# Kernel tuning notes

Hardware: AMD Instinct MI355X
Metric: run time of the kernel (lower is better)

The kernel has to match this reference:

```python
import jax, jax.numpy as jnp
import numpy as np

NUM_HEADS = 6
DIM = 192
WS = (2, 6, 12)          # window size (z, h, w)
DATA = (8, 96, 180)      # padded (plev, lat, lon)
SHIFT = (1, 3, 6)


def _position_index(ws):
    Z, H, W = ws
    zi, zj = np.arange(Z), -np.arange(Z) * Z
    hi, hj = np.arange(H), -np.arange(H) * H
    w = np.arange(W)
    c1 = np.stack(np.meshgrid(zi, hi, w, indexing='ij')).reshape(3, -1)
    c2 = np.stack(np.meshgrid(zj, hj, w, indexing='ij')).reshape(3, -1)
    coords = (c1[:, :, None] - c2[:, None, :]).transpose(1, 2, 0).copy()
    coords[:, :, 2] += W - 1
    coords[:, :, 1] *= 2 * W - 1
    coords[:, :, 0] *= (2 * W - 1) * H * H
    return coords.sum(-1).reshape(-1).astype(np.int32)


def _shift_mask(data, ws, ss):
    Z, H, W = data
    img = np.zeros((Z, H, W))
    cnt = 0
    for z in ((0, -ss[0]), (-ss[0], None)):
        for h in ((0, -ss[1]), (-ss[1], None)):
            for w in ((0, None),):  # lam=False: longitude is cyclic, no w split
                img[z[0]:z[1], h[0]:h[1], w[0]:w[1]] = cnt
                cnt += 1
    m = img.reshape(Z // ws[0], ws[0], H // ws[1], ws[1], W // ws[2], ws[2])
    m = m.transpose(0, 2, 4, 1, 3, 5).reshape(-1, ws[0] * ws[1] * ws[2])
    diff = m[:, None, :] - m[:, :, None]
    return np.where(diff != 0, -100.0, 0.0).astype(np.float32)


def setup_inputs() -> dict:
    key = jax.random.key(0)
    ks = jax.random.split(key, 4)
    N = WS[0] * WS[1] * WS[2]                      # 144 tokens / window
    nW = (DATA[0] // WS[0]) * (DATA[1] // WS[1])   # 64 (z,h) window pairs
    wlon = DATA[2] // WS[2]                        # 15 lon windows
    B_ = 1 * nW * wlon                             # 960 total windows (batch=1)
    bias_rows = (2 * WS[2] - 1) * WS[1] ** 2 * WS[0] ** 2  # 3312
    return {
        'x': jax.random.normal(ks[0], (B_, N, DIM), jnp.float32),
        'w1': jax.random.normal(ks[1], (DIM, 3 * DIM), jnp.float32) * 0.02,
        'b1': jnp.zeros((3 * DIM,), jnp.float32),
        'w2': jax.random.normal(ks[2], (DIM, DIM), jnp.float32) * 0.02,
        'b2': jnp.zeros((DIM,), jnp.float32),
        'bias_table': jax.random.normal(ks[3], (bias_rows, nW, NUM_HEADS), jnp.float32) * 0.02,
        'mask': jnp.asarray(_shift_mask(DATA, WS, SHIFT)),
        'position_index': jnp.asarray(_position_index(WS)),
        'batch_size': 1,
    }


def reference(x, w1, b1, w2, b2, bias_table, mask, position_index, batch_size):
    B_, N, C = x.shape
    Ch = C // NUM_HEADS
    scale = Ch ** -0.5
    qkv = (x @ w1 + b1).reshape(B_, N, 3, NUM_HEADS, Ch)
    qkv = jnp.transpose(qkv, (2, 0, 3, 1, 4))      # (3, B_, H, N, Ch)
    q, k, v = qkv[0] * scale, qkv[1], qkv[2]
    attn = jnp.einsum('bhnc,bhmc->bhnm', q, k)      # (B_, H, N, N)
    nW = bias_table.shape[1]
    wlon = B_ // (batch_size * nW)
    # earth-specific bias gather: (N*N,) -> (nW, H, N, N)
    bias = bias_table[position_index].reshape(N, N, nW, NUM_HEADS)
    bias = jnp.transpose(bias, (2, 3, 0, 1))
    attn = attn.reshape(batch_size, nW, wlon, NUM_HEADS, N, N) + bias[None, :, None]
    # shift mask add: (total_windows, N, N) broadcast over batch and heads
    attn = attn.reshape(batch_size, nW * wlon, NUM_HEADS, N, N) + mask[None, :, None]
    attn = jax.nn.softmax(attn.reshape(B_, NUM_HEADS, N, N), axis=-1)
    out = jnp.einsum('bhnm,bhmc->bnhc', attn, v).reshape(B_, N, C)
    return out @ w2 + b2
```

## Files before the change

kernel.cpp:

```cpp
#include <hip/hip_runtime.h>

typedef __attribute__((ext_vector_type(8))) short bf16x8;
typedef __attribute__((ext_vector_type(4))) float f32x4;
typedef unsigned short u16;
typedef unsigned int u32;

#define NTOK 144
#define CDIM 192
#define NH 6
#define CH 32
#define C3 576
#define NWIN 64
#define WLON 15
#define SCALE 0.17677669529663687f
#define LOG2E 1.4426950408889634f

#define OFF_W1T  0u
#define OFF_W2T  221184u
#define OFF_COMB 294912u
#define OFF_Q    16220160u
#define OFF_K    69304320u
#define OFF_V    122388480u

__device__ __forceinline__ u16 f2b(float f){
  u32 u = __float_as_uint(f);
  u32 r = u + 0x7FFFu + ((u >> 16) & 1u);
  return (u16)(r >> 16);
}
__device__ __forceinline__ u32 pk2(float a, float b){
  return (u32)f2b(a) | ((u32)f2b(b) << 16);
}

extern "C" __global__ __launch_bounds__(256) void prep_weights(
    const float* __restrict__ w1, const float* __restrict__ w2,
    u16* __restrict__ w1t, u16* __restrict__ w2t){
  int idx = blockIdx.x * 256 + threadIdx.x;
  if (idx < CDIM * C3){ int k = idx / C3;  int c = idx - k * C3;  w1t[c * CDIM + k] = f2b(w1[idx]); }
  if (idx < CDIM * CDIM){ int k = idx / CDIM; int c = idx - k * CDIM; w2t[c * CDIM + k] = f2b(w2[idx]); }
}

extern "C" __global__ __launch_bounds__(192) void prep_comb(
    const float* __restrict__ bt, const float* __restrict__ mask,
    const int* __restrict__ pidx, u16* __restrict__ comb){
  int nwh = blockIdx.x;
  int nw = nwh / NH, h = nwh - nw * NH;
  int tl = blockIdx.y * 192 + threadIdx.x;
  int ti = tl / 576;
  int rem = tl - ti * 576;
  int nt = rem >> 6, lane = rem & 63;
  int ib = ti * 16 + ((lane >> 4) << 2);
  int j  = nt * 16 + (lane & 15);
  const float* mrow = mask + (size_t)(nw * WLON) * (NTOK * NTOK);
  float v[4];
  #pragma unroll
  for (int r = 0; r < 4; ++r){
    int e = (ib + r) * NTOK + j;
    int pi = pidx[e];
    v[r] = (bt[((size_t)pi * NWIN + nw) * NH + h] + mrow[e]) * LOG2E;
  }
  uint2 out; out.x = pk2(v[0], v[1]); out.y = pk2(v[2], v[3]);
  *reinterpret_cast<uint2*>(comb + ((size_t)nwh * 5184 + tl) * 4) = out;
}

#define BPAD 200
extern "C" __global__ __launch_bounds__(256, 3) void qkv_gemm(
    const float* __restrict__ x, const u16* __restrict__ w1t, const float* __restrict__ b1,
    u16* __restrict__ qw, u16* __restrict__ kw, u16* __restrict__ vw){
  __shared__ u16 Bl[2][64 * BPAD];
  const int tid = threadIdx.x;
  const int wid = tid >> 6, lane = tid & 63, l15 = lane & 15, l4 = lane >> 4;
  const size_t row0 = (size_t)blockIdx.x * 128 + wid * 32;
  const f32x4 zz = {0.f, 0.f, 0.f, 0.f};

  bf16x8 af[2][6];
  #pragma unroll
  for (int mf = 0; mf < 2; ++mf){
    const float* src = x + (row0 + mf * 16 + l15) * CDIM + l4 * 8;
    #pragma unroll
    for (int kk = 0; kk < 6; ++kk){
      float4 f0 = *reinterpret_cast<const float4*>(src + kk * 32);
      float4 f1 = *reinterpret_cast<const float4*>(src + kk * 32 + 4);
      union { bf16x8 v; uint4 u; } cv;
      cv.u.x = pk2(f0.x, f0.y); cv.u.y = pk2(f0.z, f0.w);
      cv.u.z = pk2(f1.x, f1.y); cv.u.w = pk2(f1.z, f1.w);
      af[mf][kk] = cv.v;
    }
  }
  int bw_[2], n0_[2];
  #pragma unroll
  for (int mf = 0; mf < 2; ++mf){
    int t0 = (int)row0 + mf * 16 + l4 * 4;
    bw_[mf] = t0 / NTOK; n0_[mf] = t0 - bw_[mf] * NTOK;
  }

  const int sr = tid >> 2, sq = tid & 3;
  {
    const u16* src = w1t + (size_t)sr * CDIM + sq * 48;
    u16* dst = &Bl[0][sr * BPAD + sq * 48];
    #pragma unroll
    for (int i = 0; i < 48; i += 8)
      *reinterpret_cast<uint4*>(dst + i) = *reinterpret_cast<const uint4*>(src + i);
  }

  int cur = 0;
  #pragma unroll 1
  for (int nt = 0; nt < 9; ++nt){
    __syncthreads();
    if (nt < 8){
      const u16* src = w1t + (size_t)((nt + 1) * 64 + sr) * CDIM + sq * 48;
      u16* dst = &Bl[cur ^ 1][sr * BPAD + sq * 48];
      #pragma unroll
      for (int i = 0; i < 48; i += 8)
        *reinterpret_cast<uint4*>(dst + i) = *reinterpret_cast<const uint4*>(src + i);
    }
    f32x4 acc[2][4];
    #pragma unroll
    for (int mf = 0; mf < 2; ++mf)
      #pragma unroll
      for (int nf = 0; nf < 4; ++nf) acc[mf][nf] = zz;
    #pragma unroll
    for (int kk = 0; kk < 6; ++kk){
      bf16x8 bfr[4];
      #pragma unroll
      for (int nf = 0; nf < 4; ++nf)
        bfr[nf] = *reinterpret_cast<const bf16x8*>(&Bl[cur][(nf * 16 + l15) * BPAD + kk * 32 + l4 * 8]);
      #pragma unroll
      for (int mf = 0; mf < 2; ++mf)
        #pragma unroll
        for (int nf = 0; nf < 4; ++nf)
          acc[mf][nf] = __builtin_amdgcn_mfma_f32_16x16x32_bf16(af[mf][kk], bfr[nf], acc[mf][nf], 0, 0, 0);
    }
    int which = nt / 3;
    #pragma unroll
    for (int nf = 0; nf < 4; ++nf){
      int c = nt * 64 + nf * 16 + l15;
      int rem = c - which * CDIM;
      int hh = rem >> 5, chh = rem & 31;
      float bias = b1[c];
      if (which == 2){
        #pragma unroll
        for (int mf = 0; mf < 2; ++mf){
          uint2 pv;
          pv.x = pk2(acc[mf][nf][0] + bias, acc[mf][nf][1] + bias);
          pv.y = pk2(acc[mf][nf][2] + bias, acc[mf][nf][3] + bias);
          *reinterpret_cast<uint2*>(vw + (((size_t)bw_[mf] * NH + hh) * CH + chh) * NTOK + n0_[mf]) = pv;
        }
      } else {
        u16* base = (which == 0) ? qw : kw;
        float mult = (which == 0) ? (SCALE * LOG2E) : 1.0f;
        #pragma unroll
        for (int mf = 0; mf < 2; ++mf)
          #pragma unroll
          for (int r = 0; r < 4; ++r)
            base[(((size_t)bw_[mf] * NH + hh) * NTOK + n0_[mf] + r) * CH + chh] = f2b((acc[mf][nf][r] + bias) * mult);
      }
    }
    cur ^= 1;
  }
}

extern "C" __global__ __launch_bounds__(512) void attn_kernel(
    const u16* __restrict__ qw, const u16* __restrict__ kw, const u16* __restrict__ vw,
    const u16* __restrict__ comb, float* __restrict__ outbuf){
  __shared__ u16 Pl[8][16][40];
  const int tid = threadIdx.x;
  const int wv = tid >> 6, lane = tid & 63, l15 = lane & 15, l4 = lane >> 4;
  const int gw = blockIdx.x * 8 + wv;
  const int b = gw / NH, h = gw - b * NH;
  const size_t qkbase = ((size_t)b * NH + h) * (NTOK * CH);
  const size_t vbase  = ((size_t)b * NH + h) * (CH * NTOK);
  const u16* cb = comb + ((size_t)((b / WLON) * NH + h)) * (5184 * 4);
  u16* Pw = &Pl[wv][0][0];
  u32* stash32 = reinterpret_cast<u32*>(outbuf);
  const f32x4 zz = {0.f, 0.f, 0.f, 0.f};

  uint2 cc[9];
  #pragma unroll
  for (int nt = 0; nt < 9; ++nt)
    cc[nt] = *reinterpret_cast<const uint2*>(cb + ((size_t)nt * 64 + lane) * 4);

  #pragma unroll 1
  for (int ti = 0; ti < 9; ++ti){
    const int tin = (ti < 8) ? ti + 1 : ti;
    uint2 ccn[9];
    #pragma unroll
    for (int nt = 0; nt < 9; ++nt)
      ccn[nt] = *reinterpret_cast<const uint2*>(cb + ((size_t)(tin * 9 + nt) * 64 + lane) * 4);

    bf16x8 aq = *reinterpret_cast<const bf16x8*>(qw + qkbase + (ti * 16 + l15) * CH + l4 * 8);
    f32x4 s[9];
    #pragma unroll
    for (int nt = 0; nt < 9; ++nt){
      f32x4 cf;
      cf[0] = __uint_as_float(cc[nt].x << 16);
      cf[1] = __uint_as_float(cc[nt].x & 0xFFFF0000u);
      cf[2] = __uint_as_float(cc[nt].y << 16);
      cf[3] = __uint_as_float(cc[nt].y & 0xFFFF0000u);
      bf16x8 bk = *reinterpret_cast<const bf16x8*>(kw + qkbase + (nt * 16 + l15) * CH + l4 * 8);
      s[nt] = __builtin_amdgcn_mfma_f32_16x16x32_bf16(aq, bk, cf, 0, 0, 0);
    }
    float invs[4];
    #pragma unroll
    for (int r = 0; r < 4; ++r){
      float sum = 0.f;
      #pragma unroll
      for (int nt = 0; nt < 9; ++nt){
        float p = exp2f(s[nt][r]);
        s[nt][r] = p; sum += p;
      }
      #pragma unroll
      for (int off = 8; off; off >>= 1) sum += __shfl_xor(sum, off, 16);
      invs[r] = 1.0f / sum;
    }
    f32x4 oe = zz, oo = zz;
    #pragma unroll
    for (int kk = 0; kk < 5; ++kk){
      #pragma unroll
      for (int r = 0; r < 4; ++r){
        Pw[(l4 * 4 + r) * 40 + l15] = f2b(s[2 * kk][r]);
        if (kk < 4) Pw[(l4 * 4 + r) * 40 + 16 + l15] = f2b(s[2 * kk + 1][r]);
      }
      int j0 = kk * 32 + l4 * 8;
      int jc = (j0 < NTOK) ? j0 : 0;
      bf16x8 ap = *reinterpret_cast<const bf16x8*>(Pw + l15 * 40 + l4 * 8);
      bf16x8 bve = *reinterpret_cast<const bf16x8*>(vw + vbase + (size_t)(2 * l15) * NTOK + jc);
      bf16x8 bvo = *reinterpret_cast<const bf16x8*>(vw + vbase + (size_t)(2 * l15 + 1) * NTOK + jc);
      if (j0 >= NTOK) ap = bf16x8{0, 0, 0, 0, 0, 0, 0, 0};
      oe = __builtin_amdgcn_mfma_f32_16x16x32_bf16(ap, bve, oe, 0, 0, 0);
      oo = __builtin_amdgcn_mfma_f32_16x16x32_bf16(ap, bvo, oo, 0, 0, 0);
    }
    #pragma unroll
    for (int r = 0; r < 4; ++r){
      size_t t = (size_t)b * NTOK + ti * 16 + l4 * 4 + r;
      float is = invs[r];
      stash32[t * 192 + 96 + h * 16 + l15] = pk2(oe[r] * is, oo[r] * is);
    }
    #pragma unroll
    for (int nt = 0; nt < 9; ++nt) cc[nt] = ccn[nt];
  }
}

extern "C" __global__ __launch_bounds__(256, 2) void proj_gemm(
    const u16* __restrict__ w2t, const float* __restrict__ b2, float* __restrict__ outbuf){
  const int tid = threadIdx.x;
  const int wid = tid >> 6, lane = tid & 63, l15 = lane & 15, l4 = lane >> 4;
  const int hb = blockIdx.y;
  const f32x4 zz = {0.f, 0.f, 0.f, 0.f};

  bf16x8 bfr[6][6];
  #pragma unroll
  for (int nf = 0; nf < 6; ++nf)
    #pragma unroll
    for (int kk = 0; kk < 6; ++kk)
      bfr[nf][kk] = *reinterpret_cast<const bf16x8*>(
          w2t + (size_t)(hb * 96 + nf * 16 + l15) * CDIM + kk * 32 + l4 * 8);

  const u16* stash = reinterpret_cast<const u16*>(outbuf);
  const size_t rbase = (size_t)blockIdx.x * 256 + wid * 64;

#define LOADA(dst, mt) { \
    const u16* src_ = stash + (rbase + (mt) * 16 + l15) * 384 + 192 + l4 * 8; \
    _Pragma("unroll") \
    for (int kk = 0; kk < 6; ++kk) dst[kk] = *reinterpret_cast<const bf16x8*>(src_ + kk * 32); }

#define COMPUTE(a_, mt) { \
    f32x4 acc[6]; \
    _Pragma("unroll") \
    for (int nf = 0; nf < 6; ++nf) acc[nf] = zz; \
    _Pragma("unroll") \
    for (int kk = 0; kk < 6; ++kk) \
      _Pragma("unroll") \
      for (int nf = 0; nf < 6; ++nf) \
        acc[nf] = __builtin_amdgcn_mfma_f32_16x16x32_bf16(a_[kk], bfr[nf][kk], acc[nf], 0, 0, 0); \
    _Pragma("unroll") \
    for (int nf = 0; nf < 6; ++nf){ \
      int c = hb * 96 + nf * 16 + l15; \
      float bias = b2[c]; \
      _Pragma("unroll") \
      for (int r = 0; r < 4; ++r) \
        outbuf[(rbase + (mt) * 16 + l4 * 4 + r) * CDIM + c] = acc[nf][r] + bias; } }

  bf16x8 a0[6], a1[6];
  LOADA(a0, 0)
  LOADA(a1, 1) COMPUTE(a0, 0)
  LOADA(a0, 2) COMPUTE(a1, 1)
  LOADA(a1, 3) COMPUTE(a0, 2)
  COMPUTE(a1, 3)
#undef LOADA
#undef COMPUTE
}

extern "C" void kernel_launch(void* const* d_in, const int* in_sizes, int n_in,
                              void* d_out, int out_size, void* d_ws, size_t ws_size,
                              hipStream_t stream){
  const float* x    = (const float*)d_in[0];
  const float* w1   = (const float*)d_in[1];
  const float* b1   = (const float*)d_in[2];
  const float* w2   = (const float*)d_in[3];
  const float* b2   = (const float*)d_in[4];
  const float* bt   = (const float*)d_in[5];
  const float* mask = (const float*)d_in[6];
  const int*   pidx = (const int*)d_in[7];
  (void)in_sizes; (void)n_in; (void)out_size; (void)ws_size;

  char* ws = (char*)d_ws;
  u16*   w1t  = (u16*)(ws + OFF_W1T);
  u16*   w2t  = (u16*)(ws + OFF_W2T);
  u16*   comb = (u16*)(ws + OFF_COMB);
  u16*   qw   = (u16*)(ws + OFF_Q);
  u16*   kw   = (u16*)(ws + OFF_K);
  u16*   vw   = (u16*)(ws + OFF_V);
  float* out = (float*)d_out;

  prep_weights<<<dim3(432), dim3(256), 0, stream>>>(w1, w2, w1t, w2t);
  prep_comb<<<dim3(384, 27), dim3(192), 0, stream>>>(bt, mask, pidx, comb);
  qkv_gemm<<<dim3(1080), dim3(256), 0, stream>>>(x, w1t, b1, qw, kw, vw);
  attn_kernel<<<dim3(720), dim3(512), 0, stream>>>(qw, kw, vw, comb, out);
  proj_gemm<<<dim3(540, 2), dim3(256), 0, stream>>>(w2t, b2, out);
}
```

Baseline: 247.2 us.

## Pair adjacent output columns per lane in QKV GEMM and defer weight-tile LDS store

The QKV projection kernel now interleaves the B-tile rows so each lane owns two adjacent output channels, which lets Q/K writes become packed 32-bit stores instead of scattered 16-bit stores. The next weight tile is loaded from global memory into registers at the start of an iteration and written to the alternate LDS buffer only after the MFMAs and epilogue, so global load latency overlaps with compute. The cost is six extra uint4 registers per thread and a changed barrier placement.

```diff
diff --git a/kernel.cpp b/kernel.cpp
--- a/kernel.cpp
+++ b/kernel.cpp
@@ -101,60 +101,74 @@
     for (int i = 0; i < 48; i += 8)
       *reinterpret_cast<uint4*>(dst + i) = *reinterpret_cast<const uint4*>(src + i);
   }
+  __syncthreads();
 
   int cur = 0;
   #pragma unroll 1
   for (int nt = 0; nt < 9; ++nt){
-    __syncthreads();
+    uint4 ld[6];
     if (nt < 8){
       const u16* src = w1t + (size_t)((nt + 1) * 64 + sr) * CDIM + sq * 48;
-      u16* dst = &Bl[cur ^ 1][sr * BPAD + sq * 48];
-      #pragma unroll
-      for (int i = 0; i < 48; i += 8)
-        *reinterpret_cast<uint4*>(dst + i) = *reinterpret_cast<const uint4*>(src + i);
-    }
-    f32x4 acc[2][4];
-    #pragma unroll
-    for (int mf = 0; mf < 2; ++mf)
-      #pragma unroll
-      for (int nf = 0; nf < 4; ++nf) acc[mf][nf] = zz;
+      #pragma unroll
+      for (int i = 0; i < 6; ++i)
+        ld[i] = *reinterpret_cast<const uint4*>(src + i * 8);
+    }
+    f32x4 acc[4][2];
+    #pragma unroll
+    for (int f = 0; f < 4; ++f){ acc[f][0] = zz; acc[f][1] = zz; }
     #pragma unroll
     for (int kk = 0; kk < 6; ++kk){
       bf16x8 bfr[4];
       #pragma unroll
-      for (int nf = 0; nf < 4; ++nf)
-        bfr[nf] = *reinterpret_cast<const bf16x8*>(&Bl[cur][(nf * 16 + l15) * BPAD + kk * 32 + l4 * 8]);
-      #pragma unroll
-      for (int mf = 0; mf < 2; ++mf)
+      for (int f = 0; f < 4; ++f){
+        int brow = (f >> 1) * 32 + 2 * l15 + (f & 1);
+        bfr[f] = *reinterpret_cast<const bf16x8*>(&Bl[cur][brow * BPAD + kk * 32 + l4 * 8]);
+      }
+      #pragma unroll
+      for (int f = 0; f < 4; ++f)
         #pragma unroll
-        for (int nf = 0; nf < 4; ++nf)
-          acc[mf][nf] = __builtin_amdgcn_mfma_f32_16x16x32_bf16(af[mf][kk], bfr[nf], acc[mf][nf], 0, 0, 0);
+        for (int mf = 0; mf < 2; ++mf)
+          acc[f][mf] = __builtin_amdgcn_mfma_f32_16x16x32_bf16(af[mf][kk], bfr[f], acc[f][mf], 0, 0, 0);
     }
     int which = nt / 3;
     #pragma unroll
-    for (int nf = 0; nf < 4; ++nf){
-      int c = nt * 64 + nf * 16 + l15;
-      int rem = c - which * CDIM;
-      int hh = rem >> 5, chh = rem & 31;
-      float bias = b1[c];
+    for (int nf = 0; nf < 2; ++nf){
+      int cbase = nt * 64 + nf * 32;
+      int ce = cbase + 2 * l15;
+      float be = b1[ce], bo = b1[ce + 1];
+      int hh = (cbase >> 5) - which * 6;
       if (which == 2){
         #pragma unroll
         for (int mf = 0; mf < 2; ++mf){
-          uint2 pv;
-          pv.x = pk2(acc[mf][nf][0] + bias, acc[mf][nf][1] + bias);
-          pv.y = pk2(acc[mf][nf][2] + bias, acc[mf][nf][3] + bias);
-          *reinterpret_cast<uint2*>(vw + (((size_t)bw_[mf] * NH + hh) * CH + chh) * NTOK + n0_[mf]) = pv;
+          f32x4 ae = acc[nf * 2][mf], ao = acc[nf * 2 + 1][mf];
+          uint2 pe, po;
+          pe.x = pk2(ae[0] + be, ae[1] + be); pe.y = pk2(ae[2] + be, ae[3] + be);
+          po.x = pk2(ao[0] + bo, ao[1] + bo); po.y = pk2(ao[2] + bo, ao[3] + bo);
+          size_t vr = (((size_t)bw_[mf] * NH + hh) * CH + 2 * l15) * NTOK + n0_[mf];
+          *reinterpret_cast<uint2*>(vw + vr) = pe;
+          *reinterpret_cast<uint2*>(vw + vr + NTOK) = po;
         }
       } else {
         u16* base = (which == 0) ? qw : kw;
         float mult = (which == 0) ? (SCALE * LOG2E) : 1.0f;
         #pragma unroll
-        for (int mf = 0; mf < 2; ++mf)
+        for (int mf = 0; mf < 2; ++mf){
+          f32x4 ae = acc[nf * 2][mf], ao = acc[nf * 2 + 1][mf];
           #pragma unroll
-          for (int r = 0; r < 4; ++r)
-            base[(((size_t)bw_[mf] * NH + hh) * NTOK + n0_[mf] + r) * CH + chh] = f2b((acc[mf][nf][r] + bias) * mult);
+          for (int r = 0; r < 4; ++r){
+            u32 pk = pk2((ae[r] + be) * mult, (ao[r] + bo) * mult);
+            *reinterpret_cast<u32*>(base + (((size_t)bw_[mf] * NH + hh) * NTOK + n0_[mf] + r) * CH + 2 * l15) = pk;
+          }
+        }
       }
     }
+    if (nt < 8){
+      u16* dst = &Bl[cur ^ 1][sr * BPAD + sq * 48];
+      #pragma unroll
+      for (int i = 0; i < 6; ++i)
+        *reinterpret_cast<uint4*>(dst + i * 8) = ld[i];
+    }
+    __syncthreads();
     cur ^= 1;
   }
 }
```

Measured after the change: 301.5 us. +22.0%, slower.

## Fuse QKV GEMM into window attention kernel with per-head LDS weight panels

Applied to the files above, without the earlier changes.

Replaces the separate QKV GEMM and attention kernels with one kernel per window. Each block computes Q/K/V for one head into LDS and runs attention on them directly, streaming per-head weight panels into LDS with global_load_lds. This removes the large Q/K/V round trip through global memory and one launch. In exchange the weights are reloaded for every window, only 3 waves run per block, and the weight-panel prefetch is not double-buffered.

```diff
diff --git a/kernel.cpp b/kernel.cpp
--- a/kernel.cpp
+++ b/kernel.cpp
@@ -15,12 +15,12 @@
 #define SCALE 0.17677669529663687f
 #define LOG2E 1.4426950408889634f
 
-#define OFF_W1T  0u
-#define OFF_W2T  221184u
-#define OFF_COMB 294912u
-#define OFF_Q    16220160u
-#define OFF_K    69304320u
-#define OFF_V    122388480u
+#define PAN_U16 19456
+#define PANB 38912u
+
+#define OFF_W1H  0u
+#define OFF_W2T  233472u
+#define OFF_COMB 307200u
 
 __device__ __forceinline__ u16 f2b(float f){
   u32 u = __float_as_uint(f);
@@ -30,12 +30,24 @@
 __device__ __forceinline__ u32 pk2(float a, float b){
   return (u32)f2b(a) | ((u32)f2b(b) << 16);
 }
+__device__ __forceinline__ void gload_lds16(const void* g, void* l){
+  __builtin_amdgcn_global_load_lds(
+      (const __attribute__((address_space(1))) unsigned int*)g,
+      (__attribute__((address_space(3))) unsigned int*)l, 16, 0, 0);
+}
 
 extern "C" __global__ __launch_bounds__(256) void prep_weights(
     const float* __restrict__ w1, const float* __restrict__ w2,
-    u16* __restrict__ w1t, u16* __restrict__ w2t){
+    u16* __restrict__ w1hp, u16* __restrict__ w2t){
   int idx = blockIdx.x * 256 + threadIdx.x;
-  if (idx < CDIM * C3){ int k = idx / C3;  int c = idx - k * C3;  w1t[c * CDIM + k] = f2b(w1[idx]); }
+  if (idx < NH * 96 * CDIM){
+    int h = idx / (96 * CDIM);
+    int rem = idx - h * (96 * CDIM);
+    int r = rem / CDIM, k = rem - r * CDIM;
+    int which = r >> 5, sub = r & 31;
+    int col = which * CDIM + h * 32 + sub;
+    w1hp[(size_t)h * PAN_U16 + r * 200 + k] = f2b(w1[(size_t)k * C3 + col]);
+  }
   if (idx < CDIM * CDIM){ int k = idx / CDIM; int c = idx - k * CDIM; w2t[c * CDIM + k] = f2b(w2[idx]); }
 }
 
@@ -62,181 +74,167 @@
   *reinterpret_cast<uint2*>(comb + ((size_t)nwh * 5184 + tl) * 4) = out;
 }
 
-#define BPAD 200
-extern "C" __global__ __launch_bounds__(256, 3) void qkv_gemm(
-    const float* __restrict__ x, const u16* __restrict__ w1t, const float* __restrict__ b1,
-    u16* __restrict__ qw, u16* __restrict__ kw, u16* __restrict__ vw){
-  __shared__ u16 Bl[2][64 * BPAD];
+extern "C" __global__ __launch_bounds__(192) void fused_qkv_attn(
+    const float* __restrict__ x, const u16* __restrict__ w1hp, const float* __restrict__ b1,
+    const u16* __restrict__ comb, float* __restrict__ outbuf){
+  __shared__ u16 Bl[PAN_U16];
+  __shared__ u16 Ql[NTOK * 40];
+  __shared__ u16 Kl[NTOK * 40];
+  __shared__ u16 Vt[CH * 168];
+  __shared__ u16 Pl[3][16 * 40];
   const int tid = threadIdx.x;
-  const int wid = tid >> 6, lane = tid & 63, l15 = lane & 15, l4 = lane >> 4;
-  const size_t row0 = (size_t)blockIdx.x * 128 + wid * 32;
+  const int b = blockIdx.x;
+  const int nw = b / WLON;
+  const int wv = tid >> 6, lane = tid & 63, l15 = lane & 15, l4 = lane >> 4;
+  u32* stash32 = reinterpret_cast<u32*>(outbuf);
   const f32x4 zz = {0.f, 0.f, 0.f, 0.f};
 
-  bf16x8 af[2][6];
+  bf16x8 af[3][6];
+  const float* xw = x + ((size_t)b * NTOK + wv * 48 + l15) * CDIM + l4 * 8;
   #pragma unroll
-  for (int mf = 0; mf < 2; ++mf){
-    const float* src = x + (row0 + mf * 16 + l15) * CDIM + l4 * 8;
+  for (int mi = 0; mi < 3; ++mi){
     #pragma unroll
     for (int kk = 0; kk < 6; ++kk){
-      float4 f0 = *reinterpret_cast<const float4*>(src + kk * 32);
-      float4 f1 = *reinterpret_cast<const float4*>(src + kk * 32 + 4);
+      float4 f0 = *reinterpret_cast<const float4*>(xw + mi * 16 * CDIM + kk * 32);
+      float4 f1 = *reinterpret_cast<const float4*>(xw + mi * 16 * CDIM + kk * 32 + 4);
       union { bf16x8 v; uint4 u; } cv;
       cv.u.x = pk2(f0.x, f0.y); cv.u.y = pk2(f0.z, f0.w);
       cv.u.z = pk2(f1.x, f1.y); cv.u.w = pk2(f1.z, f1.w);
-      af[mf][kk] = cv.v;
-    }
-  }
-  int bw_[2], n0_[2];
-  #pragma unroll
-  for (int mf = 0; mf < 2; ++mf){
-    int t0 = (int)row0 + mf * 16 + l4 * 4;
-    bw_[mf] = t0 / NTOK; n0_[mf] = t0 - bw_[mf] * NTOK;
-  }
-
-  const int sr = tid >> 2, sq = tid & 3;
+      af[mi][kk] = cv.v;
+    }
+  }
+  for (int e = tid; e < 256; e += 192){
+    int ch = e >> 3, q = e & 7;
+    *reinterpret_cast<u32*>(Vt + ch * 168 + NTOK + q * 2) = 0u;
+  }
   {
-    const u16* src = w1t + (size_t)sr * CDIM + sq * 48;
-    u16* dst = &Bl[0][sr * BPAD + sq * 48];
-    #pragma unroll
-    for (int i = 0; i < 48; i += 8)
-      *reinterpret_cast<uint4*>(dst + i) = *reinterpret_cast<const uint4*>(src + i);
-  }
-
-  int cur = 0;
+    const char* s0 = (const char*)w1hp + lane * 16;
+    char* d0 = (char*)Bl;
+    for (int j = wv; j < 38; j += 3) gload_lds16(s0 + j * 1024, d0 + j * 1024);
+  }
+
   #pragma unroll 1
-  for (int nt = 0; nt < 9; ++nt){
+  for (int h = 0; h < NH; ++h){
     __syncthreads();
-    if (nt < 8){
-      const u16* src = w1t + (size_t)((nt + 1) * 64 + sr) * CDIM + sq * 48;
-      u16* dst = &Bl[cur ^ 1][sr * BPAD + sq * 48];
-      #pragma unroll
-      for (int i = 0; i < 48; i += 8)
-        *reinterpret_cast<uint4*>(dst + i) = *reinterpret_cast<const uint4*>(src + i);
-    }
-    f32x4 acc[2][4];
-    #pragma unroll
-    for (int mf = 0; mf < 2; ++mf)
-      #pragma unroll
-      for (int nf = 0; nf < 4; ++nf) acc[mf][nf] = zz;
+
+    f32x4 acc[3][3][2];
+    #pragma unroll
+    for (int s_ = 0; s_ < 3; ++s_)
+      #pragma unroll
+      for (int mi = 0; mi < 3; ++mi){ acc[s_][mi][0] = zz; acc[s_][mi][1] = zz; }
     #pragma unroll
     for (int kk = 0; kk < 6; ++kk){
-      bf16x8 bfr[4];
-      #pragma unroll
-      for (int nf = 0; nf < 4; ++nf)
-        bfr[nf] = *reinterpret_cast<const bf16x8*>(&Bl[cur][(nf * 16 + l15) * BPAD + kk * 32 + l4 * 8]);
-      #pragma unroll
-      for (int mf = 0; mf < 2; ++mf)
-        #pragma unroll
-        for (int nf = 0; nf < 4; ++nf)
-          acc[mf][nf] = __builtin_amdgcn_mfma_f32_16x16x32_bf16(af[mf][kk], bfr[nf], acc[mf][nf], 0, 0, 0);
-    }
-    int which = nt / 3;
-    #pragma unroll
-    for (int nf = 0; nf < 4; ++nf){
-      int c = nt * 64 + nf * 16 + l15;
-      int rem = c - which * CDIM;
-      int hh = rem >> 5, chh = rem & 31;
-      float bias = b1[c];
-      if (which == 2){
-        #pragma unroll
-        for (int mf = 0; mf < 2; ++mf){
-          uint2 pv;
-          pv.x = pk2(acc[mf][nf][0] + bias, acc[mf][nf][1] + bias);
-          pv.y = pk2(acc[mf][nf][2] + bias, acc[mf][nf][3] + bias);
-          *reinterpret_cast<uint2*>(vw + (((size_t)bw_[mf] * NH + hh) * CH + chh) * NTOK + n0_[mf]) = pv;
+      bf16x8 bf_[3][2];
+      #pragma unroll
+      for (int s_ = 0; s_ < 3; ++s_)
+        #pragma unroll
+        for (int nf = 0; nf < 2; ++nf)
+          bf_[s_][nf] = *reinterpret_cast<const bf16x8*>(
+              Bl + (s_ * 32 + nf * 16 + l15) * 200 + kk * 32 + l4 * 8);
+      #pragma unroll
+      for (int s_ = 0; s_ < 3; ++s_)
+        #pragma unroll
+        for (int mi = 0; mi < 3; ++mi)
+          #pragma unroll
+          for (int nf = 0; nf < 2; ++nf)
+            acc[s_][mi][nf] = __builtin_amdgcn_mfma_f32_16x16x32_bf16(af[mi][kk], bf_[s_][nf], acc[s_][mi][nf], 0, 0, 0);
+    }
+    float bb[3][2];
+    #pragma unroll
+    for (int s_ = 0; s_ < 3; ++s_)
+      #pragma unroll
+      for (int nf = 0; nf < 2; ++nf)
+        bb[s_][nf] = b1[s_ * CDIM + h * 32 + nf * 16 + l15];
+    #pragma unroll
+    for (int mi = 0; mi < 3; ++mi){
+      int gt0 = wv * 48 + mi * 16 + l4 * 4;
+      #pragma unroll
+      for (int nf = 0; nf < 2; ++nf){
+        int chh = nf * 16 + l15;
+        #pragma unroll
+        for (int r = 0; r < 4; ++r){
+          Ql[(gt0 + r) * 40 + chh] = f2b((acc[0][mi][nf][r] + bb[0][nf]) * (SCALE * LOG2E));
+          Kl[(gt0 + r) * 40 + chh] = f2b(acc[1][mi][nf][r] + bb[1][nf]);
         }
-      } else {
-        u16* base = (which == 0) ? qw : kw;
-        float mult = (which == 0) ? (SCALE * LOG2E) : 1.0f;
-        #pragma unroll
-        for (int mf = 0; mf < 2; ++mf)
-          #pragma unroll
-          for (int r = 0; r < 4; ++r)
-            base[(((size_t)bw_[mf] * NH + hh) * NTOK + n0_[mf] + r) * CH + chh] = f2b((acc[mf][nf][r] + bias) * mult);
-      }
-    }
-    cur ^= 1;
-  }
-}
-
-extern "C" __global__ __launch_bounds__(512) void attn_kernel(
-    const u16* __restrict__ qw, const u16* __restrict__ kw, const u16* __restrict__ vw,
-    const u16* __restrict__ comb, float* __restrict__ outbuf){
-  __shared__ u16 Pl[8][16][40];
-  const int tid = threadIdx.x;
-  const int wv = tid >> 6, lane = tid & 63, l15 = lane & 15, l4 = lane >> 4;
-  const int gw = blockIdx.x * 8 + wv;
-  const int b = gw / NH, h = gw - b * NH;
-  const size_t qkbase = ((size_t)b * NH + h) * (NTOK * CH);
-  const size_t vbase  = ((size_t)b * NH + h) * (CH * NTOK);
-  const u16* cb = comb + ((size_t)((b / WLON) * NH + h)) * (5184 * 4);
-  u16* Pw = &Pl[wv][0][0];
-  u32* stash32 = reinterpret_cast<u32*>(outbuf);
-  const f32x4 zz = {0.f, 0.f, 0.f, 0.f};
-
-  uint2 cc[9];
-  #pragma unroll
-  for (int nt = 0; nt < 9; ++nt)
-    cc[nt] = *reinterpret_cast<const uint2*>(cb + ((size_t)nt * 64 + lane) * 4);
-
-  #pragma unroll 1
-  for (int ti = 0; ti < 9; ++ti){
-    const int tin = (ti < 8) ? ti + 1 : ti;
-    uint2 ccn[9];
+        u32 v01 = pk2(acc[2][mi][nf][0] + bb[2][nf], acc[2][mi][nf][1] + bb[2][nf]);
+        u32 v23 = pk2(acc[2][mi][nf][2] + bb[2][nf], acc[2][mi][nf][3] + bb[2][nf]);
+        *reinterpret_cast<u32*>(Vt + chh * 168 + gt0)     = v01;
+        *reinterpret_cast<u32*>(Vt + chh * 168 + gt0 + 2) = v23;
+      }
+    }
+    __syncthreads();
+
+    if (h < NH - 1){
+      const char* sn = (const char*)w1hp + (size_t)(h + 1) * PANB + lane * 16;
+      char* dn = (char*)Bl;
+      for (int j = wv; j < 38; j += 3) gload_lds16(sn + j * 1024, dn + j * 1024);
+    }
+
+    const u16* cb = comb + ((size_t)(nw * NH + h)) * (5184 * 4);
+    u16* Pw = Pl[wv];
+    uint2 cc[9];
     #pragma unroll
     for (int nt = 0; nt < 9; ++nt)
-      ccn[nt] = *reinterpret_cast<const uint2*>(cb + ((size_t)(tin * 9 + nt) * 64 + lane) * 4);
-
-    bf16x8 aq = *reinterpret_cast<const bf16x8*>(qw + qkbase + (ti * 16 + l15) * CH + l4 * 8);
-    f32x4 s[9];
-    #pragma unroll
-    for (int nt = 0; nt < 9; ++nt){
-      f32x4 cf;
-      cf[0] = __uint_as_float(cc[nt].x << 16);
-      cf[1] = __uint_as_float(cc[nt].x & 0xFFFF0000u);
-      cf[2] = __uint_as_float(cc[nt].y << 16);
-      cf[3] = __uint_as_float(cc[nt].y & 0xFFFF0000u);
-      bf16x8 bk = *reinterpret_cast<const bf16x8*>(kw + qkbase + (nt * 16 + l15) * CH + l4 * 8);
-      s[nt] = __builtin_amdgcn_mfma_f32_16x16x32_bf16(aq, bk, cf, 0, 0, 0);
-    }
-    float invs[4];
-    #pragma unroll
-    for (int r = 0; r < 4; ++r){
-      float sum = 0.f;
+      cc[nt] = *reinterpret_cast<const uint2*>(cb + ((size_t)((wv * 3) * 9 + nt) * 64 + lane) * 4);
+    #pragma unroll 1
+    for (int mi = 0; mi < 3; ++mi){
+      const int ti = wv * 3 + mi;
+      const int tin = (mi < 2) ? ti + 1 : ti;
+      uint2 ccn[9];
+      #pragma unroll
+      for (int nt = 0; nt < 9; ++nt)
+        ccn[nt] = *reinterpret_cast<const uint2*>(cb + ((size_t)(tin * 9 + nt) * 64 + lane) * 4);
+
+      bf16x8 aq = *reinterpret_cast<const bf16x8*>(Ql + (ti * 16 + l15) * 40 + l4 * 8);
+      f32x4 s[9];
       #pragma unroll
       for (int nt = 0; nt < 9; ++nt){
-        float p = exp2f(s[nt][r]);
-        s[nt][r] = p; sum += p;
-      }
-      #pragma unroll
-      for (int off = 8; off; off >>= 1) sum += __shfl_xor(sum, off, 16);
-      invs[r] = 1.0f / sum;
-    }
-    f32x4 oe = zz, oo = zz;
-    #pragma unroll
-    for (int kk = 0; kk < 5; ++kk){
+        f32x4 cf;
+        cf[0] = __uint_as_float(cc[nt].x << 16);
+        cf[1] = __uint_as_float(cc[nt].x & 0xFFFF0000u);
+        cf[2] = __uint_as_float(cc[nt].y << 16);
+        cf[3] = __uint_as_float(cc[nt].y & 0xFFFF0000u);
+        bf16x8 bk = *reinterpret_cast<const bf16x8*>(Kl + (nt * 16 + l15) * 40 + l4 * 8);
+        s[nt] = __builtin_amdgcn_mfma_f32_16x16x32_bf16(aq, bk, cf, 0, 0, 0);
+      }
+      float invs[4];
       #pragma unroll
       for (int r = 0; r < 4; ++r){
-        Pw[(l4 * 4 + r) * 40 + l15] = f2b(s[2 * kk][r]);
-        if (kk < 4) Pw[(l4 * 4 + r) * 40 + 16 + l15] = f2b(s[2 * kk + 1][r]);
-      }
-      int j0 = kk * 32 + l4 * 8;
-      int jc = (j0 < NTOK) ? j0 : 0;
-      bf16x8 ap = *reinterpret_cast<const bf16x8*>(Pw + l15 * 40 + l4 * 8);
-      bf16x8 bve = *reinterpret_cast<const bf16x8*>(vw + vbase + (size_t)(2 * l15) * NTOK + jc);
-      bf16x8 bvo = *reinterpret_cast<const bf16x8*>(vw + vbase + (size_t)(2 * l15 + 1) * NTOK + jc);
-      if (j0 >= NTOK) ap = bf16x8{0, 0, 0, 0, 0, 0, 0, 0};
-      oe = __builtin_amdgcn_mfma_f32_16x16x32_bf16(ap, bve, oe, 0, 0, 0);
-      oo = __builtin_amdgcn_mfma_f32_16x16x32_bf16(ap, bvo, oo, 0, 0, 0);
-    }
-    #pragma unroll
-    for (int r = 0; r < 4; ++r){
-      size_t t = (size_t)b * NTOK + ti * 16 + l4 * 4 + r;
-      float is = invs[r];
-      stash32[t * 192 + 96 + h * 16 + l15] = pk2(oe[r] * is, oo[r] * is);
-    }
-    #pragma unroll
-    for (int nt = 0; nt < 9; ++nt) cc[nt] = ccn[nt];
+        float sum = 0.f;
+        #pragma unroll
+        for (int nt = 0; nt < 9; ++nt){
+          float p = exp2f(s[nt][r]);
+          s[nt][r] = p; sum += p;
+        }
+        #pragma unroll
+        for (int off = 8; off; off >>= 1) sum += __shfl_xor(sum, off, 16);
+        invs[r] = 1.0f / sum;
+      }
+      f32x4 oe = zz, oo = zz;
+      #pragma unroll
+      for (int kk = 0; kk < 5; ++kk){
+        #pragma unroll
+        for (int r = 0; r < 4; ++r){
+          Pw[(l4 * 4 + r) * 40 + l15] = f2b(s[2 * kk][r]);
+          if (kk < 4) Pw[(l4 * 4 + r) * 40 + 16 + l15] = f2b(s[2 * kk + 1][r]);
+        }
+        int j0 = kk * 32 + l4 * 8;
+        bf16x8 ap  = *reinterpret_cast<const bf16x8*>(Pw + l15 * 40 + l4 * 8);
+        bf16x8 bve = *reinterpret_cast<const bf16x8*>(Vt + (2 * l15) * 168 + j0);
+        bf16x8 bvo = *reinterpret_cast<const bf16x8*>(Vt + (2 * l15 + 1) * 168 + j0);
+        if (j0 >= NTOK) ap = bf16x8{0, 0, 0, 0, 0, 0, 0, 0};
+        oe = __builtin_amdgcn_mfma_f32_16x16x32_bf16(ap, bve, oe, 0, 0, 0);
+        oo = __builtin_amdgcn_mfma_f32_16x16x32_bf16(ap, bvo, oo, 0, 0, 0);
+      }
+      #pragma unroll
+      for (int r = 0; r < 4; ++r){
+        size_t t = (size_t)b * NTOK + ti * 16 + l4 * 4 + r;
+        float is = invs[r];
+        stash32[t * 192 + 96 + h * 16 + l15] = pk2(oe[r] * is, oo[r] * is);
+      }
+      #pragma unroll
+      for (int nt = 0; nt < 9; ++nt) cc[nt] = ccn[nt];
+    }
   }
 }
 
@@ -304,17 +302,13 @@
   (void)in_sizes; (void)n_in; (void)out_size; (void)ws_size;
 
   char* ws = (char*)d_ws;
-  u16*   w1t  = (u16*)(ws + OFF_W1T);
+  u16*   w1hp = (u16*)(ws + OFF_W1H);
   u16*   w2t  = (u16*)(ws + OFF_W2T);
   u16*   comb = (u16*)(ws + OFF_COMB);
-  u16*   qw   = (u16*)(ws + OFF_Q);
-  u16*   kw   = (u16*)(ws + OFF_K);
-  u16*   vw   = (u16*)(ws + OFF_V);
   float* out = (float*)d_out;
 
-  prep_weights<<<dim3(432), dim3(256), 0, stream>>>(w1, w2, w1t, w2t);
+  prep_weights<<<dim3(432), dim3(256), 0, stream>>>(w1, w2, w1hp, w2t);
   prep_comb<<<dim3(384, 27), dim3(192), 0, stream>>>(bt, mask, pidx, comb);
-  qkv_gemm<<<dim3(1080), dim3(256), 0, stream>>>(x, w1t, b1, qw, kw, vw);
-  attn_kernel<<<dim3(720), dim3(512), 0, stream>>>(qw, kw, vw, comb, out);
+  fused_qkv_attn<<<dim3(960), dim3(192), 0, stream>>>(x, w1hp, b1, comb, out);
   proj_gemm<<<dim3(540, 2), dim3(256), 0, stream>>>(w2t, b2, out);
 }
```

Result: slower. 318.3 us (+28.7%).
